# Performance work log

Measured on AMD Instinct MI355X. Metric: run time of the kernel, lower is better.

## Reference

```python
import jax, jax.numpy as jnp
import numpy as np

N_NODES = 65536
D_FEAT = 64
N_EDGES = 1048576


def setup_inputs() -> dict:
    key = jax.random.key(0)
    ks = jax.random.split(key, 8)
    x1 = jax.random.normal(ks[0], (N_NODES, D_FEAT), dtype=jnp.float32)
    x2 = jax.random.normal(ks[1], (N_NODES, D_FEAT), dtype=jnp.float32)
    a1_rows = jax.random.randint(ks[2], (N_EDGES,), 0, N_NODES, dtype=jnp.int32)
    a1_cols = jax.random.randint(ks[3], (N_EDGES,), 0, N_NODES, dtype=jnp.int32)
    a1_vals = jax.random.uniform(ks[4], (N_EDGES,), dtype=jnp.float32)
    a2_rows = jax.random.randint(ks[5], (N_EDGES,), 0, N_NODES, dtype=jnp.int32)
    a2_cols = jax.random.randint(ks[6], (N_EDGES,), 0, N_NODES, dtype=jnp.int32)
    a2_vals = jax.random.uniform(ks[7], (N_EDGES,), dtype=jnp.float32)
    return {
        "x1": x1, "x2": x2,
        "a1_rows": a1_rows, "a1_cols": a1_cols, "a1_vals": a1_vals,
        "a2_rows": a2_rows, "a2_cols": a2_cols, "a2_vals": a2_vals,
    }


def _spmm(rows, cols, vals, x, n_rows):
    # COO SpMM: out[r] = sum_{e: rows[e]==r} vals[e] * x[cols[e]]
    gathered = vals[:, None] * x[cols]            # [E, D]
    return jax.ops.segment_sum(gathered, rows, num_segments=n_rows)


def reference(x1, x2, a1_rows, a1_cols, a1_vals, a2_rows, a2_cols, a2_vals):
    out1 = _spmm(a1_rows, a1_cols, a1_vals, x1, N_NODES)
    out2 = _spmm(a2_rows, a2_cols, a2_vals, x2, N_NODES)
    return (out1, out2)
```

## Files before the change

kernel.cpp:

```cpp
#include <hip/hip_runtime.h>
#include <hip/hip_bf16.h>

#define N_NODES 65536
#define D_FEAT  64
#define N_EDGES 1048576
#define NBUCK   512
#define ROWS_PB 128
#define BCAP    2560
#define EPB     8192
#define XH_ELEMS ((size_t)N_NODES * D_FEAT)

static __device__ __forceinline__ unsigned short f2bf(float f) {
    unsigned b = __float_as_uint(f);
    return (unsigned short)((b + 0x7fffu + ((b >> 16) & 1u)) >> 16);
}
static __device__ __forceinline__ float bf2f(unsigned short u) {
    return __uint_as_float(((unsigned)u) << 16);
}

__global__ __launch_bounds__(256) void cvt_kernel(
    const float* __restrict__ x1, const float* __restrict__ x2,
    unsigned short* __restrict__ xh)
{
    const size_t half = XH_ELEMS / 4;
    const size_t base = (size_t)blockIdx.x * 1024;
    #pragma unroll
    for (int k = 0; k < 4; ++k) {
        size_t i = base + (size_t)k * 256 + threadIdx.x;
        float4 f = (i < half) ? ((const float4*)x1)[i]
                              : ((const float4*)x2)[i - half];
        ushort4 o;
        o.x = f2bf(f.x); o.y = f2bf(f.y); o.z = f2bf(f.z); o.w = f2bf(f.w);
        ((ushort4*)xh)[i] = o;
    }
}

__global__ __launch_bounds__(1024) void bin_kernel(
    const int* __restrict__ r1, const int* __restrict__ c1, const float* __restrict__ v1,
    const int* __restrict__ r2, const int* __restrict__ c2, const float* __restrict__ v2,
    int*   __restrict__ gcursor,
    uint2* __restrict__ perm)
{
    __shared__ uint2 ent[EPB];
    __shared__ unsigned short binof[EPB];
    __shared__ int hist[NBUCK];
    __shared__ int offs[NBUCK];
    __shared__ int cur[NBUCK];
    __shared__ int gbase[NBUCK];

    const int tid = threadIdx.x;
    const int mat = blockIdx.x >> 7;
    const int lb  = blockIdx.x & 127;
    const int*   rows = mat ? r2 : r1;
    const int*   cols = mat ? c2 : c1;
    const float* vals = mat ? v2 : v1;
    int*   gcur = gcursor + mat * NBUCK;
    uint2* pm   = perm + (size_t)mat * NBUCK * BCAP;

    for (int i = tid; i < NBUCK; i += 1024) hist[i] = 0;
    __syncthreads();

    const int base_e = lb * EPB;
    int r[8], c[8];
    float v[8];
    *(int4*)&r[0]   = ((const int4*)(rows + base_e))[tid * 2];
    *(int4*)&r[4]   = ((const int4*)(rows + base_e))[tid * 2 + 1];
    *(int4*)&c[0]   = ((const int4*)(cols + base_e))[tid * 2];
    *(int4*)&c[4]   = ((const int4*)(cols + base_e))[tid * 2 + 1];
    *(float4*)&v[0] = ((const float4*)(vals + base_e))[tid * 2];
    *(float4*)&v[4] = ((const float4*)(vals + base_e))[tid * 2 + 1];

    #pragma unroll
    for (int k = 0; k < 8; ++k) atomicAdd(&hist[r[k] >> 7], 1);
    __syncthreads();

    int my = (tid < NBUCK) ? hist[tid] : 0;
    if (tid < NBUCK) offs[tid] = my;
    __syncthreads();
    for (int off = 1; off < NBUCK; off <<= 1) {
        int add = 0;
        if (tid < NBUCK && tid >= off) add = offs[tid - off];
        __syncthreads();
        if (tid < NBUCK) offs[tid] += add;
        __syncthreads();
    }
    if (tid < NBUCK) {
        int excl = offs[tid] - my;
        offs[tid] = excl;
        cur[tid]  = excl;
        gbase[tid] = atomicAdd(&gcur[tid], my);
    }
    __syncthreads();

    #pragma unroll
    for (int k = 0; k < 8; ++k) {
        const int b = r[k] >> 7;
        const int pos = atomicAdd(&cur[b], 1);
        uint2 e;
        e.x = __float_as_uint(v[k]);
        e.y = ((unsigned)c[k] << 7) | ((unsigned)r[k] & 127u);
        ent[pos]   = e;
        binof[pos] = (unsigned short)b;
    }
    __syncthreads();

    for (int i = tid; i < EPB; i += 1024) {
        const int b   = binof[i];
        const int idx = gbase[b] + (i - offs[b]);
        if (idx < BCAP) pm[(size_t)b * BCAP + idx] = ent[i];
    }
}

__global__ __launch_bounds__(1024, 4) void spmm_kernel(
    const int*            __restrict__ gcursor,
    const uint2*          __restrict__ perm,
    const unsigned short* __restrict__ xh,
    float*                __restrict__ out)
{
    __shared__ uint2 ent[BCAP];
    __shared__ int   hist[ROWS_PB];
    __shared__ int   offs[ROWS_PB + 1];
    __shared__ int   cur[ROWS_PB];
    __shared__ int   stmp[ROWS_PB];

    const int gb  = blockIdx.x;
    const int mat = gb >> 9;
    const int b   = gb & 511;
    const int tid = threadIdx.x;

    const uint2* pbase = perm + ((size_t)mat * NBUCK + b) * BCAP;
    const unsigned short* xm = xh + (size_t)mat * XH_ELEMS;
    float* ob = out + (size_t)mat * XH_ELEMS + (size_t)b * ROWS_PB * D_FEAT;

    const int cnt = min(gcursor[mat * NBUCK + b], BCAP);

    if (tid < ROWS_PB) hist[tid] = 0;
    __syncthreads();

    uint2 mine[3];
    int nm = 0;
    for (int i = tid; i < cnt; i += 1024) {
        uint2 e = pbase[i];
        mine[nm++] = e;
        atomicAdd(&hist[e.y & (ROWS_PB - 1)], 1);
    }
    __syncthreads();

    if (tid < ROWS_PB) stmp[tid] = hist[tid];
    __syncthreads();
    for (int off = 1; off < ROWS_PB; off <<= 1) {
        int vv = 0;
        if (tid < ROWS_PB && tid >= off) vv = stmp[tid - off];
        __syncthreads();
        if (tid < ROWS_PB) stmp[tid] += vv;
        __syncthreads();
    }
    if (tid < ROWS_PB) {
        int excl = stmp[tid] - hist[tid];
        offs[tid] = excl;
        cur[tid]  = excl;
    }
    if (tid == 0) offs[ROWS_PB] = cnt;
    __syncthreads();

    for (int k = 0; k < nm; ++k) {
        int r   = mine[k].y & (ROWS_PB - 1);
        int pos = atomicAdd(&cur[r], 1);
        ent[pos] = mine[k];
    }
    __syncthreads();

    const int wave = tid >> 6;
    const int lane = tid & 63;
    const int sub  = lane >> 4;
    const int fl   = lane & 15;

#define GBODY(EE) {                                                          \
        uint2 en = ent[(EE) + sub];                                          \
        float vv = __uint_as_float(en.x);                                    \
        ushort4 q = *(const ushort4*)(xm + (((size_t)(en.y >> 7)) << 6)      \
                                         + (fl << 2));                       \
        acc.x = fmaf(vv, bf2f(q.x), acc.x);                                  \
        acc.y = fmaf(vv, bf2f(q.y), acc.y);                                  \
        acc.z = fmaf(vv, bf2f(q.z), acc.z);                                  \
        acc.w = fmaf(vv, bf2f(q.w), acc.w); }

    #pragma unroll
    for (int rr = 0; rr < 8; ++rr) {
        const int r   = wave * 8 + rr;
        int e         = offs[r];
        const int end = offs[r + 1];
        float4 acc = make_float4(0.f, 0.f, 0.f, 0.f);

        for (; e + 16 <= end; e += 16) {
            GBODY(e) GBODY(e + 4) GBODY(e + 8) GBODY(e + 12)
        }
        for (; e + 4 <= end; e += 4) { GBODY(e) }
        if (e < end) {
            int  idx = e + sub;
            bool ok  = idx < end;
            uint2 en = ent[ok ? idx : (end - 1)];
            float vv = ok ? __uint_as_float(en.x) : 0.f;
            ushort4 q = *(const ushort4*)(xm + (((size_t)(en.y >> 7)) << 6)
                                             + (fl << 2));
            acc.x = fmaf(vv, bf2f(q.x), acc.x);
            acc.y = fmaf(vv, bf2f(q.y), acc.y);
            acc.z = fmaf(vv, bf2f(q.z), acc.z);
            acc.w = fmaf(vv, bf2f(q.w), acc.w);
        }

        acc.x += __shfl_xor(acc.x, 16); acc.y += __shfl_xor(acc.y, 16);
        acc.z += __shfl_xor(acc.z, 16); acc.w += __shfl_xor(acc.w, 16);
        acc.x += __shfl_xor(acc.x, 32); acc.y += __shfl_xor(acc.y, 32);
        acc.z += __shfl_xor(acc.z, 32); acc.w += __shfl_xor(acc.w, 32);

        if (lane < 16)
            *(float4*)(ob + r * D_FEAT + (fl << 2)) = acc;
    }
#undef GBODY
}

__global__ __launch_bounds__(256) void spmm_atomic_kernel(
    const float* __restrict__ x,
    const int*   __restrict__ rows,
    const int*   __restrict__ cols,
    const float* __restrict__ vals,
    float*       __restrict__ out,
    int n_edges)
{
    const int gid  = blockIdx.x * blockDim.x + threadIdx.x;
    const int edge = gid >> 6;
    const int lane = threadIdx.x & 63;
    if (edge >= n_edges) return;
    const int   r = rows[edge];
    const int   c = cols[edge];
    const float v = vals[edge];
    atomicAdd(&out[(size_t)r * D_FEAT + lane], v * x[(size_t)c * D_FEAT + lane]);
}

extern "C" void kernel_launch(void* const* d_in, const int* in_sizes, int n_in,
                              void* d_out, int out_size, void* d_ws, size_t ws_size,
                              hipStream_t stream) {
    const float* x1      = (const float*)d_in[0];
    const float* x2      = (const float*)d_in[1];
    const int*   a1_rows = (const int*)  d_in[2];
    const int*   a1_cols = (const int*)  d_in[3];
    const float* a1_vals = (const float*)d_in[4];
    const int*   a2_rows = (const int*)  d_in[5];
    const int*   a2_cols = (const int*)  d_in[6];
    const float* a2_vals = (const float*)d_in[7];

    float* out  = (float*)d_out;
    float* out1 = out;
    float* out2 = out + XH_ELEMS;

    int*   gcur = (int*)d_ws;
    uint2* perm = (uint2*)(gcur + 2 * NBUCK);
    unsigned short* xh = (unsigned short*)(perm + (size_t)2 * NBUCK * BCAP);

    const size_t needed = 2 * NBUCK * sizeof(int)
                        + (size_t)2 * NBUCK * BCAP * sizeof(uint2)
                        + (size_t)2 * XH_ELEMS * sizeof(short);

    if (ws_size < needed) {
        hipMemsetAsync(d_out, 0, (size_t)out_size * sizeof(float), stream);
        const int blocks = (N_EDGES * 64 + 255) / 256;
        spmm_atomic_kernel<<<blocks, 256, 0, stream>>>(x1, a1_rows, a1_cols, a1_vals, out1, N_EDGES);
        spmm_atomic_kernel<<<blocks, 256, 0, stream>>>(x2, a2_rows, a2_cols, a2_vals, out2, N_EDGES);
        return;
    }

    hipMemsetAsync(gcur, 0, 2 * NBUCK * sizeof(int), stream);

    cvt_kernel<<<2048, 256, 0, stream>>>(x1, x2, xh);

    bin_kernel<<<2 * (N_EDGES / EPB), 1024, 0, stream>>>(
        a1_rows, a1_cols, a1_vals, a2_rows, a2_cols, a2_vals, gcur, perm);

    spmm_kernel<<<2 * NBUCK, 1024, 0, stream>>>(gcur, perm, xh, out);
}
```

Before: 185.1 us.

## Fuse bf16 conversion into bin kernel, use wave-shuffle scans and 16-byte gathers

```diff
diff --git a/kernel.cpp b/kernel.cpp
--- a/kernel.cpp
+++ b/kernel.cpp
@@ -14,28 +14,19 @@
     unsigned b = __float_as_uint(f);
     return (unsigned short)((b + 0x7fffu + ((b >> 16) & 1u)) >> 16);
 }
-static __device__ __forceinline__ float bf2f(unsigned short u) {
-    return __uint_as_float(((unsigned)u) << 16);
-}
-
-__global__ __launch_bounds__(256) void cvt_kernel(
+
+static __device__ __forceinline__ int wave_incl_scan(int v, int lane) {
+    #pragma unroll
+    for (int d = 1; d < 64; d <<= 1) {
+        int t = __shfl_up(v, d, 64);
+        if (lane >= d) v += t;
+    }
+    return v;
+}
+
+__global__ __launch_bounds__(1024) void bin_kernel(
     const float* __restrict__ x1, const float* __restrict__ x2,
-    unsigned short* __restrict__ xh)
-{
-    const size_t half = XH_ELEMS / 4;
-    const size_t base = (size_t)blockIdx.x * 1024;
-    #pragma unroll
-    for (int k = 0; k < 4; ++k) {
-        size_t i = base + (size_t)k * 256 + threadIdx.x;
-        float4 f = (i < half) ? ((const float4*)x1)[i]
-                              : ((const float4*)x2)[i - half];
-        ushort4 o;
-        o.x = f2bf(f.x); o.y = f2bf(f.y); o.z = f2bf(f.z); o.w = f2bf(f.w);
-        ((ushort4*)xh)[i] = o;
-    }
-}
-
-__global__ __launch_bounds__(1024) void bin_kernel(
+    unsigned short* __restrict__ xh,
     const int* __restrict__ r1, const int* __restrict__ c1, const float* __restrict__ v1,
     const int* __restrict__ r2, const int* __restrict__ c2, const float* __restrict__ v2,
     int*   __restrict__ gcursor,
@@ -47,18 +38,19 @@
     __shared__ int offs[NBUCK];
     __shared__ int cur[NBUCK];
     __shared__ int gbase[NBUCK];
-
-    const int tid = threadIdx.x;
-    const int mat = blockIdx.x >> 7;
-    const int lb  = blockIdx.x & 127;
+    __shared__ int wsum[8];
+
+    const int tid  = threadIdx.x;
+    const int lane = tid & 63;
+    const int wv   = tid >> 6;
+    const int mat  = blockIdx.x >> 7;
+    const int lb   = blockIdx.x & 127;
     const int*   rows = mat ? r2 : r1;
     const int*   cols = mat ? c2 : c1;
     const float* vals = mat ? v2 : v1;
-    int*   gcur = gcursor + mat * NBUCK;
-    uint2* pm   = perm + (size_t)mat * NBUCK * BCAP;
+    uint2* pm = perm + (size_t)mat * NBUCK * BCAP;
 
     for (int i = tid; i < NBUCK; i += 1024) hist[i] = 0;
-    __syncthreads();
 
     const int base_e = lb * EPB;
     int r[8], c[8];
@@ -70,25 +62,40 @@
     *(float4*)&v[0] = ((const float4*)(vals + base_e))[tid * 2];
     *(float4*)&v[4] = ((const float4*)(vals + base_e))[tid * 2 + 1];
 
+    {
+        const size_t half  = XH_ELEMS / 4;
+        const size_t cbase = (size_t)blockIdx.x * 8192;
+        #pragma unroll
+        for (int k = 0; k < 8; ++k) {
+            size_t i = cbase + (size_t)k * 1024 + tid;
+            float4 f = (i < half) ? ((const float4*)x1)[i]
+                                  : ((const float4*)x2)[i - half];
+            ushort4 o;
+            o.x = f2bf(f.x); o.y = f2bf(f.y); o.z = f2bf(f.z); o.w = f2bf(f.w);
+            ((ushort4*)xh)[i] = o;
+        }
+    }
+
+    __syncthreads();
     #pragma unroll
     for (int k = 0; k < 8; ++k) atomicAdd(&hist[r[k] >> 7], 1);
     __syncthreads();
 
-    int my = (tid < NBUCK) ? hist[tid] : 0;
-    if (tid < NBUCK) offs[tid] = my;
-    __syncthreads();
-    for (int off = 1; off < NBUCK; off <<= 1) {
+    int my = 0, incl = 0;
+    if (wv < 8) {
+        my   = hist[tid];
+        incl = wave_incl_scan(my, lane);
+        if (lane == 63) wsum[wv] = incl;
+    }
+    __syncthreads();
+    if (wv < 8) {
         int add = 0;
-        if (tid < NBUCK && tid >= off) add = offs[tid - off];
-        __syncthreads();
-        if (tid < NBUCK) offs[tid] += add;
-        __syncthreads();
-    }
-    if (tid < NBUCK) {
-        int excl = offs[tid] - my;
+        #pragma unroll
+        for (int w = 0; w < 8; ++w) if (w < wv) add += wsum[w];
+        const int excl = incl - my + add;
         offs[tid] = excl;
         cur[tid]  = excl;
-        gbase[tid] = atomicAdd(&gcur[tid], my);
+        gbase[tid] = atomicAdd(&gcursor[mat * NBUCK + tid], my);
     }
     __syncthreads();
 
@@ -111,7 +118,7 @@
     }
 }
 
-__global__ __launch_bounds__(1024, 4) void spmm_kernel(
+__global__ __launch_bounds__(1024, 8) void spmm_kernel(
     const int*            __restrict__ gcursor,
     const uint2*          __restrict__ perm,
     const unsigned short* __restrict__ xh,
@@ -121,12 +128,14 @@
     __shared__ int   hist[ROWS_PB];
     __shared__ int   offs[ROWS_PB + 1];
     __shared__ int   cur[ROWS_PB];
-    __shared__ int   stmp[ROWS_PB];
-
-    const int gb  = blockIdx.x;
-    const int mat = gb >> 9;
-    const int b   = gb & 511;
-    const int tid = threadIdx.x;
+    __shared__ int   wscr[2];
+
+    const int gb   = blockIdx.x;
+    const int mat  = gb >> 9;
+    const int b    = gb & 511;
+    const int tid  = threadIdx.x;
+    const int lane = tid & 63;
+    const int wave = tid >> 6;
 
     const uint2* pbase = perm + ((size_t)mat * NBUCK + b) * BCAP;
     const unsigned short* xm = xh + (size_t)mat * XH_ELEMS;
@@ -146,17 +155,15 @@
     }
     __syncthreads();
 
-    if (tid < ROWS_PB) stmp[tid] = hist[tid];
-    __syncthreads();
-    for (int off = 1; off < ROWS_PB; off <<= 1) {
-        int vv = 0;
-        if (tid < ROWS_PB && tid >= off) vv = stmp[tid - off];
-        __syncthreads();
-        if (tid < ROWS_PB) stmp[tid] += vv;
-        __syncthreads();
-    }
-    if (tid < ROWS_PB) {
-        int excl = stmp[tid] - hist[tid];
+    int my = 0, incl = 0;
+    if (wave < 2) {
+        my   = hist[tid];
+        incl = wave_incl_scan(my, lane);
+        if (lane == 63) wscr[wave] = incl;
+    }
+    __syncthreads();
+    if (wave < 2) {
+        const int excl = incl - my + (wave == 1 ? wscr[0] : 0);
         offs[tid] = excl;
         cur[tid]  = excl;
     }
@@ -164,60 +171,83 @@
     __syncthreads();
 
     for (int k = 0; k < nm; ++k) {
-        int r   = mine[k].y & (ROWS_PB - 1);
-        int pos = atomicAdd(&cur[r], 1);
+        int rr  = mine[k].y & (ROWS_PB - 1);
+        int pos = atomicAdd(&cur[rr], 1);
         ent[pos] = mine[k];
     }
     __syncthreads();
 
-    const int wave = tid >> 6;
-    const int lane = tid & 63;
-    const int sub  = lane >> 4;
-    const int fl   = lane & 15;
-
-#define GBODY(EE) {                                                          \
+    const int sub = lane >> 3;
+    const int fl  = lane & 7;
+
+#define GB(ACC, EE) {                                                        \
         uint2 en = ent[(EE) + sub];                                          \
         float vv = __uint_as_float(en.x);                                    \
-        ushort4 q = *(const ushort4*)(xm + (((size_t)(en.y >> 7)) << 6)      \
-                                         + (fl << 2));                       \
-        acc.x = fmaf(vv, bf2f(q.x), acc.x);                                  \
-        acc.y = fmaf(vv, bf2f(q.y), acc.y);                                  \
-        acc.z = fmaf(vv, bf2f(q.z), acc.z);                                  \
-        acc.w = fmaf(vv, bf2f(q.w), acc.w); }
+        const uint4 q = *(const uint4*)(xm + (((size_t)(en.y >> 7)) << 6)    \
+                                           + (fl << 3));                     \
+        ACC[0] = fmaf(vv, __uint_as_float(q.x << 16),         ACC[0]);       \
+        ACC[1] = fmaf(vv, __uint_as_float(q.x & 0xffff0000u), ACC[1]);       \
+        ACC[2] = fmaf(vv, __uint_as_float(q.y << 16),         ACC[2]);       \
+        ACC[3] = fmaf(vv, __uint_as_float(q.y & 0xffff0000u), ACC[3]);       \
+        ACC[4] = fmaf(vv, __uint_as_float(q.z << 16),         ACC[4]);       \
+        ACC[5] = fmaf(vv, __uint_as_float(q.z & 0xffff0000u), ACC[5]);       \
+        ACC[6] = fmaf(vv, __uint_as_float(q.w << 16),         ACC[6]);       \
+        ACC[7] = fmaf(vv, __uint_as_float(q.w & 0xffff0000u), ACC[7]); }
+
+#define GBM(ACC, EE, END) {                                                  \
+        const int idx = (EE) + sub;                                          \
+        const bool ok = idx < (END);                                         \
+        uint2 en = ent[ok ? idx : (END) - 1];                                \
+        float vv = ok ? __uint_as_float(en.x) : 0.f;                         \
+        const uint4 q = *(const uint4*)(xm + (((size_t)(en.y >> 7)) << 6)    \
+                                           + (fl << 3));                     \
+        ACC[0] = fmaf(vv, __uint_as_float(q.x << 16),         ACC[0]);       \
+        ACC[1] = fmaf(vv, __uint_as_float(q.x & 0xffff0000u), ACC[1]);       \
+        ACC[2] = fmaf(vv, __uint_as_float(q.y << 16),         ACC[2]);       \
+        ACC[3] = fmaf(vv, __uint_as_float(q.y & 0xffff0000u), ACC[3]);       \
+        ACC[4] = fmaf(vv, __uint_as_float(q.z << 16),         ACC[4]);       \
+        ACC[5] = fmaf(vv, __uint_as_float(q.z & 0xffff0000u), ACC[5]);       \
+        ACC[6] = fmaf(vv, __uint_as_float(q.w << 16),         ACC[6]);       \
+        ACC[7] = fmaf(vv, __uint_as_float(q.w & 0xffff0000u), ACC[7]); }
 
     #pragma unroll
-    for (int rr = 0; rr < 8; ++rr) {
-        const int r   = wave * 8 + rr;
-        int e         = offs[r];
-        const int end = offs[r + 1];
-        float4 acc = make_float4(0.f, 0.f, 0.f, 0.f);
-
-        for (; e + 16 <= end; e += 16) {
-            GBODY(e) GBODY(e + 4) GBODY(e + 8) GBODY(e + 12)
+    for (int rp = 0; rp < 8; rp += 2) {
+        const int rA = wave * 8 + rp;
+        const int rB = rA + 1;
+        int eA = offs[rA]; const int endA = offs[rA + 1];
+        int eB = endA;     const int endB = offs[rB + 1];
+
+        float a[8]  = {0.f, 0.f, 0.f, 0.f, 0.f, 0.f, 0.f, 0.f};
+        float bq[8] = {0.f, 0.f, 0.f, 0.f, 0.f, 0.f, 0.f, 0.f};
+
+        while (eA + 8 <= endA && eB + 8 <= endB) {
+            GB(a, eA) GB(bq, eB)
+            eA += 8; eB += 8;
         }
-        for (; e + 4 <= end; e += 4) { GBODY(e) }
-        if (e < end) {
-            int  idx = e + sub;
-            bool ok  = idx < end;
-            uint2 en = ent[ok ? idx : (end - 1)];
-            float vv = ok ? __uint_as_float(en.x) : 0.f;
-            ushort4 q = *(const ushort4*)(xm + (((size_t)(en.y >> 7)) << 6)
-                                             + (fl << 2));
-            acc.x = fmaf(vv, bf2f(q.x), acc.x);
-            acc.y = fmaf(vv, bf2f(q.y), acc.y);
-            acc.z = fmaf(vv, bf2f(q.z), acc.z);
-            acc.w = fmaf(vv, bf2f(q.w), acc.w);
+        while (eA + 8 <= endA) { GB(a, eA)  eA += 8; }
+        while (eB + 8 <= endB) { GB(bq, eB) eB += 8; }
+        if (eA < endA) GBM(a, eA, endA)
+        if (eB < endB) GBM(bq, eB, endB)
+
+        #pragma unroll
+        for (int i = 0; i < 8; ++i) {
+            a[i]  += __shfl_xor(a[i],  8);
+            a[i]  += __shfl_xor(a[i],  16);
+            a[i]  += __shfl_xor(a[i],  32);
+            bq[i] += __shfl_xor(bq[i], 8);
+            bq[i] += __shfl_xor(bq[i], 16);
+            bq[i] += __shfl_xor(bq[i], 32);
         }
 
-        acc.x += __shfl_xor(acc.x, 16); acc.y += __shfl_xor(acc.y, 16);
-        acc.z += __shfl_xor(acc.z, 16); acc.w += __shfl_xor(acc.w, 16);
-        acc.x += __shfl_xor(acc.x, 32); acc.y += __shfl_xor(acc.y, 32);
-        acc.z += __shfl_xor(acc.z, 32); acc.w += __shfl_xor(acc.w, 32);
-
-        if (lane < 16)
-            *(float4*)(ob + r * D_FEAT + (fl << 2)) = acc;
-    }
-#undef GBODY
+        if (lane < 8) {
+            *(float4*)(ob + rA * D_FEAT + (fl << 3))     = make_float4(a[0], a[1], a[2], a[3]);
+            *(float4*)(ob + rA * D_FEAT + (fl << 3) + 4) = make_float4(a[4], a[5], a[6], a[7]);
+            *(float4*)(ob + rB * D_FEAT + (fl << 3))     = make_float4(bq[0], bq[1], bq[2], bq[3]);
+            *(float4*)(ob + rB * D_FEAT + (fl << 3) + 4) = make_float4(bq[4], bq[5], bq[6], bq[7]);
+        }
+    }
+#undef GB
+#undef GBM
 }
 
 __global__ __launch_bounds__(256) void spmm_atomic_kernel(
@@ -272,9 +302,8 @@
 
     hipMemsetAsync(gcur, 0, 2 * NBUCK * sizeof(int), stream);
 
-    cvt_kernel<<<2048, 256, 0, stream>>>(x1, x2, xh);
-
     bin_kernel<<<2 * (N_EDGES / EPB), 1024, 0, stream>>>(
+        x1, x2, xh,
         a1_rows, a1_cols, a1_vals, a2_rows, a2_cols, a2_vals, gcur, perm);
 
     spmm_kernel<<<2 * NBUCK, 1024, 0, stream>>>(gcur, perm, xh, out);
```

After: 188.2 us. No clear change (+1.7%).
